# Kernel optimization log

Measured on AMD Instinct MI355X. Metric: run time of the kernel, lower is better.

The kernel has to match this reference:

```python
import jax, jax.numpy as jnp
import numpy as np

CELL_SIDE = 0.5
GRID_N = 6
HIDDEN = 128


def setup_inputs() -> dict:
    key = jax.random.key(0)
    k1, k2, k3 = jax.random.split(key, 3)
    N = 8192
    obs = jax.random.normal(k1, (N, 2), dtype=jnp.float32)          # agent (x, y) positions
    W = jax.random.normal(k2, (HIDDEN, GRID_N * GRID_N), dtype=jnp.float32) * 0.1  # Linear weight
    b = jax.random.normal(k3, (HIDDEN,), dtype=jnp.float32) * 0.1   # Linear bias
    return {"obs": obs, "W": W, "b": b}


def reference(obs, W, b):
    # Vectorized equivalent of per-agent occupancy + Linear embedding.
    N = obs.shape[0]
    g = GRID_N
    # relative grid coordinates of agent j w.r.t. agent i: [N, N, 2]
    rel = (obs[None, :, :] - obs[:, None, :]) / CELL_SIDE + g / 2.0
    # validity: both coords in [0, g), j != i, neither position is NaN
    in_range = jnp.all((rel >= 0) & (rel < g), axis=-1)             # [N, N]
    not_self = ~jnp.eye(N, dtype=bool)
    valid = ~jnp.isnan(obs[:, 0])                                   # [N]
    w = (in_range & not_self & valid[None, :] & valid[:, None]).astype(obs.dtype)
    # integer cell indices (floor == trunc since valid rel >= 0); clip keeps masked-out
    # (weight 0) entries in-bounds for the scatter.
    ij = jnp.floor(rel).astype(jnp.int32)
    cell = jnp.clip(ij[..., 0], 0, g - 1) * g + jnp.clip(ij[..., 1], 0, g - 1)  # [N, N]
    flat_idx = (jnp.arange(N, dtype=jnp.int32)[:, None] * (g * g) + cell).reshape(-1)
    occ = jnp.zeros((N * g * g,), obs.dtype).at[flat_idx].add(w.reshape(-1))
    occ = occ.reshape(N, g * g)                                     # [N, 36]
    return occ @ W.T + b                                            # [N, 128]
```

## Files before the change

### kernel.cpp

```cpp
#include <hip/hip_runtime.h>

#define NAGENT 8192
#define NCELL 36
#define HIDDEN 128
#define CSTRIDE 37
#define PWORDS 18
#define NROWS 64
#define NCHUNK 16
#define JCHUNK (NAGENT / NCHUNK)

typedef float v2f __attribute__((ext_vector_type(2)));

__global__ __launch_bounds__(256) void occ_hist_kernel(
    const float2* __restrict__ obs, unsigned* __restrict__ partial) {
  __shared__ unsigned cnt[NROWS * 64];
  const int tid  = threadIdx.x;
  const int lane = tid & 63;
  const int wv   = tid >> 6;

#pragma unroll
  for (int k = tid; k < NROWS * 64; k += 256) cnt[k] = 0u;
  __syncthreads();

  const int agent = blockIdx.y * 64 + lane;
  const float2 oi = obs[agent];
  const v2f two = {2.0f, 2.0f};
  const v2f cxy = {fmaf(oi.x, -2.0f, 3.0f), fmaf(oi.y, -2.0f, 3.0f)};
  unsigned* base = cnt + 9 * 64 + lane;

  const int jbeg = blockIdx.x * JCHUNK + wv * (JCHUNK / 4);
  const float4* jp = (const float4*)obs + (jbeg >> 1);

#pragma unroll 8
  for (int t = 0; t < JCHUNK / 8; ++t) {
    const float4 o2 = jp[t];
    {
      const v2f p = {o2.x, o2.y};
      const v2f r = __builtin_elementwise_fma(p, two, cxy);
      const int ux = (int)__builtin_floorf(__builtin_amdgcn_fmed3f(r.x, -1.0f, 6.0f));
      const int uy = (int)__builtin_floorf(__builtin_amdgcn_fmed3f(r.y, -1.0f, 6.0f));
      atomicAdd(&base[(ux * 8 + uy) * 64], 1u);
    }
    {
      const v2f p = {o2.z, o2.w};
      const v2f r = __builtin_elementwise_fma(p, two, cxy);
      const int ux = (int)__builtin_floorf(__builtin_amdgcn_fmed3f(r.x, -1.0f, 6.0f));
      const int uy = (int)__builtin_floorf(__builtin_amdgcn_fmed3f(r.y, -1.0f, 6.0f));
      atomicAdd(&base[(ux * 8 + uy) * 64], 1u);
    }
  }
  __syncthreads();

  unsigned* gbase = partial + (size_t)blockIdx.x * PWORDS * NAGENT +
                    (size_t)blockIdx.y * 64;
  for (int k = tid; k < PWORDS * 64; k += 256) {
    const int w = k >> 6, l = k & 63;
    const int c0 = 2 * w, c1 = 2 * w + 1;
    const int r0 = (c0 / 6 + 1) * 8 + (c0 % 6 + 1);
    const int r1 = (c1 / 6 + 1) * 8 + (c1 % 6 + 1);
    gbase[(size_t)w * NAGENT + l] = cnt[r0 * 64 + l] | (cnt[r1 * 64 + l] << 16);
  }
}

__global__ __launch_bounds__(256) void occ_gemm_kernel(
    const unsigned* __restrict__ partial, const float* __restrict__ W,
    const float* __restrict__ bias, float* __restrict__ out) {
  __shared__ float Wl[HIDDEN * NCELL];
  __shared__ float occ[16 * CSTRIDE];
  const int tid = threadIdx.x;

  const float4* W4 = (const float4*)W;
  float4* Wl4 = (float4*)Wl;
  for (int k = tid; k < HIDDEN * NCELL / 4; k += 256) Wl4[k] = W4[k];

  const int agBase = blockIdx.x * 16;
  for (int k = tid; k < 16 * PWORDS; k += 256) {
    const int a = k & 15, w = k >> 4;
    const unsigned* p = partial + (size_t)w * NAGENT + agBase + a;
    unsigned s = 0;
#pragma unroll
    for (int c = 0; c < NCHUNK; ++c) s += p[(size_t)c * PWORDS * NAGENT];
    float lo = (float)(s & 0xFFFFu);
    float hi = (float)(s >> 16);
    if (w == 10) hi -= 1.0f;
    occ[a * CSTRIDE + 2 * w]     = lo;
    occ[a * CSTRIDE + 2 * w + 1] = hi;
  }
  __syncthreads();

  const int a  = tid >> 4;
  const int hg = tid & 15;

  float occf[NCELL];
#pragma unroll
  for (int c = 0; c < NCELL; ++c) occf[c] = occ[a * CSTRIDE + c];

  float acc[8];
#pragma unroll
  for (int k = 0; k < 8; ++k) acc[k] = bias[hg + 16 * k];

#pragma unroll
  for (int c4 = 0; c4 < 9; ++c4) {
#pragma unroll
    for (int k = 0; k < 8; ++k) {
      const float4 w4 = *(const float4*)&Wl[(hg + 16 * k) * NCELL + c4 * 4];
      acc[k] = fmaf(occf[4 * c4 + 0], w4.x, acc[k]);
      acc[k] = fmaf(occf[4 * c4 + 1], w4.y, acc[k]);
      acc[k] = fmaf(occf[4 * c4 + 2], w4.z, acc[k]);
      acc[k] = fmaf(occf[4 * c4 + 3], w4.w, acc[k]);
    }
  }

  float* ob = out + (size_t)(agBase + a) * HIDDEN;
#pragma unroll
  for (int k = 0; k < 8; ++k) ob[hg + 16 * k] = acc[k];
}

extern "C" void kernel_launch(void* const* d_in, const int* in_sizes, int n_in,
                              void* d_out, int out_size, void* d_ws, size_t ws_size,
                              hipStream_t stream) {
  (void)in_sizes; (void)n_in; (void)out_size; (void)ws_size;
  const float2* obs = (const float2*)d_in[0];
  const float*  W   = (const float*)d_in[1];
  const float*  b   = (const float*)d_in[2];
  float* out = (float*)d_out;
  unsigned* partial = (unsigned*)d_ws;

  occ_hist_kernel<<<dim3(NCHUNK, 128), dim3(256), 0, stream>>>(obs, partial);
  occ_gemm_kernel<<<dim3(512), dim3(256), 0, stream>>>(partial, W, b, out);
}
```

Before: 89.48 us.

## Bucket-sort agents spatially and cull distant neighbor blocks via bounding boxes

Adds a three-kernel counting sort that orders agents into a 16x16 grid of spatial buckets and records their original indices. The histogram kernel then works on the sorted positions. Each wave computes a bounding box for its 64 target agents and for each 16-agent source block, and skips any source block that cannot land within the 6x6 neighborhood. The GEMM kernel writes results back through the stored permutation. The aim is to avoid most of the all-pairs atomic histogram work, at the cost of extra launches, a memset and an unordered output write pattern.

```diff
diff --git a/kernel.cpp b/kernel.cpp
--- a/kernel.cpp
+++ b/kernel.cpp
@@ -8,11 +8,54 @@
 #define NROWS 64
 #define NCHUNK 16
 #define JCHUNK (NAGENT / NCHUNK)
+#define MARGIN 1.501f
 
 typedef float v2f __attribute__((ext_vector_type(2)));
 
+#define WS_PARTIAL 0
+#define WS_BCNT (NCHUNK * PWORDS * NAGENT)
+#define WS_BCUR (WS_BCNT + 256)
+#define WS_SIDX (WS_BCUR + 256)
+#define WS_SOBS (WS_SIDX + NAGENT)
+
+__device__ __forceinline__ int bucket_of(float2 o) {
+  int bx = (int)__builtin_floorf((o.x + 4.0f) * 2.0f);
+  int by = (int)__builtin_floorf((o.y + 4.0f) * 2.0f);
+  bx = min(max(bx, 0), 15); by = min(max(by, 0), 15);
+  return bx * 16 + by;
+}
+
+__global__ __launch_bounds__(256) void sort_count(
+    const float2* __restrict__ obs, unsigned* __restrict__ bcnt) {
+  const int a = blockIdx.x * 256 + threadIdx.x;
+  atomicAdd(&bcnt[bucket_of(obs[a])], 1u);
+}
+
+__global__ __launch_bounds__(256) void sort_scan(
+    const unsigned* __restrict__ bcnt, unsigned* __restrict__ bcur) {
+  __shared__ unsigned sh[256];
+  const int tid = threadIdx.x;
+  const unsigned x = bcnt[tid];
+  sh[tid] = x; __syncthreads();
+  for (int off = 1; off < 256; off <<= 1) {
+    unsigned v = (tid >= off) ? sh[tid - off] : 0u;
+    __syncthreads(); sh[tid] += v; __syncthreads();
+  }
+  bcur[tid] = sh[tid] - x;
+}
+
+__global__ __launch_bounds__(256) void sort_scatter(
+    const float2* __restrict__ obs, unsigned* __restrict__ bcur,
+    unsigned* __restrict__ sidx, float2* __restrict__ sobs) {
+  const int a = blockIdx.x * 256 + threadIdx.x;
+  const float2 o = obs[a];
+  const unsigned pos = atomicAdd(&bcur[bucket_of(o)], 1u);
+  sidx[pos] = (unsigned)a;
+  sobs[pos] = o;
+}
+
 __global__ __launch_bounds__(256) void occ_hist_kernel(
-    const float2* __restrict__ obs, unsigned* __restrict__ partial) {
+    const float2* __restrict__ sobs, unsigned* __restrict__ partial) {
   __shared__ unsigned cnt[NROWS * 64];
   const int tid  = threadIdx.x;
   const int lane = tid & 63;
@@ -23,30 +66,58 @@
   __syncthreads();
 
   const int agent = blockIdx.y * 64 + lane;
-  const float2 oi = obs[agent];
+  const float2 oi = sobs[agent];
   const v2f two = {2.0f, 2.0f};
   const v2f cxy = {fmaf(oi.x, -2.0f, 3.0f), fmaf(oi.y, -2.0f, 3.0f)};
   unsigned* base = cnt + 9 * 64 + lane;
 
+  float gxmin = oi.x, gxmax = oi.x, gymin = oi.y, gymax = oi.y;
+#pragma unroll
+  for (int m = 1; m < 64; m <<= 1) {
+    gxmin = fminf(gxmin, __shfl_xor(gxmin, m));
+    gxmax = fmaxf(gxmax, __shfl_xor(gxmax, m));
+    gymin = fminf(gymin, __shfl_xor(gymin, m));
+    gymax = fmaxf(gymax, __shfl_xor(gymax, m));
+  }
+
   const int jbeg = blockIdx.x * JCHUNK + wv * (JCHUNK / 4);
-  const float4* jp = (const float4*)obs + (jbeg >> 1);
-
-#pragma unroll 8
-  for (int t = 0; t < JCHUNK / 8; ++t) {
-    const float4 o2 = jp[t];
-    {
-      const v2f p = {o2.x, o2.y};
-      const v2f r = __builtin_elementwise_fma(p, two, cxy);
-      const int ux = (int)__builtin_floorf(__builtin_amdgcn_fmed3f(r.x, -1.0f, 6.0f));
-      const int uy = (int)__builtin_floorf(__builtin_amdgcn_fmed3f(r.y, -1.0f, 6.0f));
-      atomicAdd(&base[(ux * 8 + uy) * 64], 1u);
+  const float4* jp = (const float4*)sobs + (jbeg >> 1);
+  {
+    const float4 v = jp[lane];
+    float bxmin = fminf(v.x, v.z), bxmax = fmaxf(v.x, v.z);
+    float bymin = fminf(v.y, v.w), bymax = fmaxf(v.y, v.w);
+#pragma unroll
+    for (int m = 1; m < 8; m <<= 1) {
+      bxmin = fminf(bxmin, __shfl_xor(bxmin, m));
+      bxmax = fmaxf(bxmax, __shfl_xor(bxmax, m));
+      bymin = fminf(bymin, __shfl_xor(bymin, m));
+      bymax = fmaxf(bymax, __shfl_xor(bymax, m));
     }
-    {
-      const v2f p = {o2.z, o2.w};
-      const v2f r = __builtin_elementwise_fma(p, two, cxy);
-      const int ux = (int)__builtin_floorf(__builtin_amdgcn_fmed3f(r.x, -1.0f, 6.0f));
-      const int uy = (int)__builtin_floorf(__builtin_amdgcn_fmed3f(r.y, -1.0f, 6.0f));
-      atomicAdd(&base[(ux * 8 + uy) * 64], 1u);
+    const bool ok = !(bxmin > gxmax + MARGIN || bxmax < gxmin - MARGIN ||
+                      bymin > gymax + MARGIN || bymax < gymin - MARGIN);
+    const unsigned long long mask = __ballot(ok);
+
+    for (int k = 0; k < 8; ++k) {
+      if (!((mask >> (8 * k)) & 1ull)) continue;
+      const float4* bp = jp + 8 * k;
+#pragma unroll
+      for (int t = 0; t < 8; ++t) {
+        const float4 o2 = bp[t];
+        {
+          const v2f p = {o2.x, o2.y};
+          const v2f r = __builtin_elementwise_fma(p, two, cxy);
+          const int ux = (int)__builtin_floorf(__builtin_amdgcn_fmed3f(r.x, -1.0f, 6.0f));
+          const int uy = (int)__builtin_floorf(__builtin_amdgcn_fmed3f(r.y, -1.0f, 6.0f));
+          atomicAdd(&base[(ux * 8 + uy) * 64], 1u);
+        }
+        {
+          const v2f p = {o2.z, o2.w};
+          const v2f r = __builtin_elementwise_fma(p, two, cxy);
+          const int ux = (int)__builtin_floorf(__builtin_amdgcn_fmed3f(r.x, -1.0f, 6.0f));
+          const int uy = (int)__builtin_floorf(__builtin_amdgcn_fmed3f(r.y, -1.0f, 6.0f));
+          atomicAdd(&base[(ux * 8 + uy) * 64], 1u);
+        }
+      }
     }
   }
   __syncthreads();
@@ -63,8 +134,9 @@
 }
 
 __global__ __launch_bounds__(256) void occ_gemm_kernel(
-    const unsigned* __restrict__ partial, const float* __restrict__ W,
-    const float* __restrict__ bias, float* __restrict__ out) {
+    const unsigned* __restrict__ partial, const unsigned* __restrict__ sidx,
+    const float* __restrict__ W, const float* __restrict__ bias,
+    float* __restrict__ out) {
   __shared__ float Wl[HIDDEN * NCELL];
   __shared__ float occ[16 * CSTRIDE];
   const int tid = threadIdx.x;
@@ -111,7 +183,7 @@
     }
   }
 
-  float* ob = out + (size_t)(agBase + a) * HIDDEN;
+  float* ob = out + (size_t)sidx[agBase + a] * HIDDEN;
 #pragma unroll
   for (int k = 0; k < 8; ++k) ob[hg + 16 * k] = acc[k];
 }
@@ -124,8 +196,17 @@
   const float*  W   = (const float*)d_in[1];
   const float*  b   = (const float*)d_in[2];
   float* out = (float*)d_out;
-  unsigned* partial = (unsigned*)d_ws;
-
-  occ_hist_kernel<<<dim3(NCHUNK, 128), dim3(256), 0, stream>>>(obs, partial);
-  occ_gemm_kernel<<<dim3(512), dim3(256), 0, stream>>>(partial, W, b, out);
-}
+  unsigned* ws = (unsigned*)d_ws;
+  unsigned* partial = ws + WS_PARTIAL;
+  unsigned* bcnt = ws + WS_BCNT;
+  unsigned* bcur = ws + WS_BCUR;
+  unsigned* sidx = ws + WS_SIDX;
+  float2*   sobs = (float2*)(ws + WS_SOBS);
+
+  hipMemsetAsync(bcnt, 0, 256 * sizeof(unsigned), stream);
+  sort_count  <<<dim3(32), dim3(256), 0, stream>>>(obs, bcnt);
+  sort_scan   <<<dim3(1),  dim3(256), 0, stream>>>(bcnt, bcur);
+  sort_scatter<<<dim3(32), dim3(256), 0, stream>>>(obs, bcur, sidx, sobs);
+  occ_hist_kernel<<<dim3(NCHUNK, 128), dim3(256), 0, stream>>>(sobs, partial);
+  occ_gemm_kernel<<<dim3(512), dim3(256), 0, stream>>>(partial, sidx, W, b, out);
+}
```

After: 115.7 us. +29.3%, slower.
